# Performance work log

Hardware: AMD Instinct MI355X
Metric: run time of the kernel (lower is better)

## Reference

```python
import jax, jax.numpy as jnp
import numpy as np

NEG_RATIO = 5          # neg_sample_ratio, also k (num_nodes-1 >> ratio)
THRESH = 0.7           # hard_neg_threshold
SMOOTH = 0.1           # label_smoothing
NUM_NODES = 200_000
DIM = 128
B = 1024               # batch size, all labels == 1 (all positives)
FILL_VAL = -1.0e9


def _l2_normalize(x, eps=1e-12):
    # F.normalize(p=2, dim=-1): divide by clamped L2 norm
    n = jnp.sqrt(jnp.sum(x * x, axis=-1, keepdims=True))
    return x / jnp.maximum(n, eps)


def setup_inputs() -> dict:
    key = jax.random.key(0)
    k1, k2, k3, k4 = jax.random.split(key, 4)
    src_nodes = jax.random.randint(k1, (B,), 0, NUM_NODES)
    dst_nodes = jax.random.randint(k2, (B,), 0, NUM_NODES)
    labels = jnp.ones((B,), dtype=jnp.float32)  # all positives -> pos_mask all True
    timestamps = jax.random.uniform(k3, (B,), dtype=jnp.float32)
    memory = jax.random.normal(k4, (NUM_NODES, DIM), dtype=jnp.float32)
    return {
        "src_nodes": src_nodes,
        "dst_nodes": dst_nodes,
        "labels": labels,
        "timestamps": timestamps,
        "memory": memory,
    }


def reference(src_nodes, dst_nodes, labels, timestamps, memory):
    # --- embedding gather + L2 normalize ---
    src_emb = memory[src_nodes]                      # [B, D]
    s = _l2_normalize(src_emb).astype(jnp.float16)   # use_half_precision=True
    c = _l2_normalize(memory).astype(jnp.float16)    # [N, D]

    # --- similarity [B, N], back to fp32 ---
    sim = jnp.matmul(s, c.T).astype(jnp.float32)

    # --- mask out ground-truth dst and below-threshold sims ---
    cols = jnp.arange(NUM_NODES)
    allowed = cols[None, :] != dst_nodes[:, None]    # exclude GT positives
    valid = allowed & (sim > THRESH)
    score = jnp.where(valid, sim, FILL_VAL)

    # --- top-k hard negatives per positive ---
    k = NEG_RATIO  # min(neg_sample_ratio, num_nodes-1)
    topk_vals, topk_idx = jax.lax.top_k(score, k)    # [B, k]
    is_real = (topk_vals > FILL_VAL + 1.0).reshape(-1)  # [B*k]

    # --- fallback random negatives (fixed-shape equivalent of the torch
    #     pack-real-then-pad-random assembly; total count == B*k either way) ---
    rkey = jax.random.key(42)
    rand_dst = jax.random.randint(rkey, (B * k,), 0, NUM_NODES)
    src_rep = jnp.repeat(src_nodes, k)               # [B*k]
    rand_dst = jnp.where(rand_dst == src_rep, (rand_dst + 1) % NUM_NODES, rand_dst)

    final_src = src_rep
    final_dst = jnp.where(is_real, topk_idx.reshape(-1), rand_dst)
    neg_ts = jnp.repeat(timestamps, k)

    # --- assemble augmented batch ---
    new_src = jnp.concatenate([src_nodes, final_src])
    new_dst = jnp.concatenate([dst_nodes, final_dst])
    new_labels = jnp.concatenate([labels, jnp.zeros((B * k,), labels.dtype)])
    new_ts = jnp.concatenate([timestamps, neg_ts])

    # --- label smoothing ---
    new_labels = new_labels * (1.0 - SMOOTH) + (1.0 - new_labels) * SMOOTH

    return new_src, new_dst, new_labels, new_ts, topk_vals
```

## Files before the change

### kernel.cpp

```cpp
#include <hip/hip_runtime.h>

#define NUM_NODES 200000
#define DIM 128
#define BATCH 1024
#define K_NEG 5
#define CAP 16
#define NBLK 250
#define CPB 800
#define TCOL 32
#define NT 25
#define THRESH 0.7f
#define FILL (-1.0e9f)

typedef __attribute__((ext_vector_type(8))) short short8;
typedef __attribute__((ext_vector_type(16))) float f32x16;

__device__ __forceinline__ unsigned short f2bf(float x) {
  unsigned u = __builtin_bit_cast(unsigned, x);
  return (unsigned short)((u + 0x7fffu + ((u >> 16) & 1u)) >> 16);
}

__device__ __forceinline__ void stage16(const void* g, void* l) {
  __builtin_amdgcn_global_load_lds(
      (const __attribute__((address_space(1))) unsigned int*)g,
      (__attribute__((address_space(3))) unsigned int*)l,
      16, 0, 0);
}

__device__ __forceinline__ void tf2x32(unsigned k0, unsigned k1,
                                       unsigned x0, unsigned x1,
                                       unsigned* o0, unsigned* o1) {
  unsigned ks2 = k0 ^ k1 ^ 0x1BD11BDAu;
  unsigned v0 = x0 + k0, v1 = x1 + k1;
#define TFR(r) { v0 += v1; v1 = (v1 << r) | (v1 >> (32 - r)); v1 ^= v0; }
  TFR(13) TFR(15) TFR(26) TFR(6)   v0 += k1;  v1 += ks2 + 1u;
  TFR(17) TFR(29) TFR(16) TFR(24)  v0 += ks2; v1 += k0 + 2u;
  TFR(13) TFR(15) TFR(26) TFR(6)   v0 += k0;  v1 += k1 + 3u;
  TFR(17) TFR(29) TFR(16) TFR(24)  v0 += k1;  v1 += ks2 + 4u;
  TFR(13) TFR(15) TFR(26) TFR(6)   v0 += ks2; v1 += k0 + 5u;
#undef TFR
  *o0 = v0; *o1 = v1;
}

__device__ __forceinline__ unsigned rbits32(unsigned ka, unsigned kb, unsigned m) {
  unsigned o0, o1;
  tf2x32(ka, kb, 0u, m, &o0, &o1);
  return o0 ^ o1;
}

__global__ void prep_kernel(const float* __restrict__ memory,
                            const int* __restrict__ src_nodes,
                            unsigned short* __restrict__ s16f,
                            int* __restrict__ cand_cnt) {
  int tid = threadIdx.x;
  int gid = blockIdx.x * 256 + tid;
  if (gid < BATCH) cand_cnt[gid] = 0;
  int row = blockIdx.x * 4 + (tid >> 6);
  int L = tid & 63;
  int s = src_nodes[row];
  float2 v = ((const float2*)(memory + (size_t)s * DIM))[L];
  float ss = v.x * v.x + v.y * v.y;
#pragma unroll
  for (int off = 32; off > 0; off >>= 1) ss += __shfl_xor(ss, off);
  float inv = 1.0f / fmaxf(sqrtf(ss), 1e-12f);
  unsigned p = (unsigned)f2bf(v.x * inv) | ((unsigned)f2bf(v.y * inv) << 16);
  int ms = row >> 5, l32 = row & 31;
  int c = L >> 2;
  int ks = c >> 1, half = c & 1;
  ((unsigned*)s16f)[(((ms * 8 + ks) * 64) + half * 32 + l32) * 4 + (L & 3)] = p;
}

__global__ __launch_bounds__(512, 2) void sim_scan_kernel(
    const float* __restrict__ memory,
    const unsigned short* __restrict__ s16f,
    const int* __restrict__ dst_nodes,
    int* __restrict__ cand_cnt,
    float* __restrict__ cand_val,
    int* __restrict__ cand_idx) {
  __shared__ char qbuf[8][2048];
  __shared__ unsigned short fragb[2][4096];
  __shared__ float nrmb[2][32];

  int tid = threadIdx.x;
  int wid = tid >> 6;
  int lane = tid & 63;
  int half = lane >> 5;
  int l32 = lane & 31;
  int jb0 = blockIdx.x * CPB;

  int ccol = wid * 4 + (lane & 3);
  int cseg = lane >> 2;

  const char* mb = (const char*)memory;

#define QSTAGE(t) {                                                             \
    const char* g = mb + (size_t)(jb0 + (t) * TCOL + ccol) * 512 + (cseg << 5); \
    stage16(g, &qbuf[wid][0]);                                                  \
    stage16(g + 16, &qbuf[wid][1024]);                                          \
  }

#define QCONVERT(p) {                                                           \
    asm volatile("s_waitcnt vmcnt(0)" ::: "memory");                            \
    __builtin_amdgcn_sched_barrier(0);                                          \
    float4 q0 = *(const float4*)(&qbuf[wid][lane << 4]);                        \
    float4 q1 = *(const float4*)(&qbuf[wid][1024 + (lane << 4)]);               \
    float ss = q0.x * q0.x + q0.y * q0.y + q0.z * q0.z + q0.w * q0.w            \
             + q1.x * q1.x + q1.y * q1.y + q1.z * q1.z + q1.w * q1.w;           \
    ss += __shfl_xor(ss, 4); ss += __shfl_xor(ss, 8);                           \
    ss += __shfl_xor(ss, 16); ss += __shfl_xor(ss, 32);                         \
    short8 f;                                                                   \
    f[0] = (short)f2bf(q0.x); f[1] = (short)f2bf(q0.y);                         \
    f[2] = (short)f2bf(q0.z); f[3] = (short)f2bf(q0.w);                         \
    f[4] = (short)f2bf(q1.x); f[5] = (short)f2bf(q1.y);                         \
    f[6] = (short)f2bf(q1.z); f[7] = (short)f2bf(q1.w);                         \
    *(short8*)((char*)fragb[p] + ((cseg * 32 + (ccol ^ (cseg & 7))) << 4)) = f; \
    if (cseg == 0) nrmb[p][ccol] = fmaxf(sqrtf(ss), 1e-12f);                    \
  }

  QSTAGE(0);
  const short8* __restrict__ af = (const short8*)s16f;
  short8 a[4][8];
#pragma unroll
  for (int m = 0; m < 4; ++m)
#pragma unroll
    for (int ks = 0; ks < 8; ++ks)
      a[m][ks] = af[(((wid * 4 + m) * 8) + ks) * 64 + lane];
  QCONVERT(0);
  __syncthreads();

  f32x16 Z;
#pragma unroll
  for (int i = 0; i < 16; ++i) Z[i] = 0.0f;

  for (int t = 0; t < NT; ++t) {
    int par = t & 1;

    if (t + 1 < NT) QSTAGE(t + 1);

    float nv = nrmb[par][l32];
    float thr = THRESH * nv;
    float invv = 1.0f / nv;
    int gj = jb0 + t * TCOL + l32;
    short8 bf[8];
#pragma unroll
    for (int ks = 0; ks < 8; ++ks) {
      int s0 = 2 * ks + half;
      bf[ks] = *(const short8*)((char*)fragb[par] + ((s0 * 32 + (l32 ^ (s0 & 7))) << 4));
    }

#pragma unroll
    for (int mp = 0; mp < 2; ++mp) {
      f32x16 accA = __builtin_amdgcn_mfma_f32_32x32x16_bf16(a[mp * 2][0], bf[0], Z, 0, 0, 0);
      f32x16 accB = __builtin_amdgcn_mfma_f32_32x32x16_bf16(a[mp * 2 + 1][0], bf[0], Z, 0, 0, 0);
#pragma unroll
      for (int ks = 1; ks < 8; ++ks) {
        accA = __builtin_amdgcn_mfma_f32_32x32x16_bf16(a[mp * 2][ks], bf[ks], accA, 0, 0, 0);
        accB = __builtin_amdgcn_mfma_f32_32x32x16_bf16(a[mp * 2 + 1][ks], bf[ks], accB, 0, 0, 0);
      }
      float mA = accA[0], mB = accB[0];
#pragma unroll
      for (int i = 1; i < 16; ++i) { mA = fmaxf(mA, accA[i]); mB = fmaxf(mB, accB[i]); }
      if (mA > thr || mB > thr) {
#pragma unroll
        for (int e = 0; e < 2; ++e) {
#pragma unroll
          for (int r = 0; r < 16; ++r) {
            float raw = (e == 0) ? accA[r] : accB[r];
            if (raw > thr) {
              int gi = (wid * 4 + mp * 2 + e) * 32 + (r & 3) + 8 * (r >> 2) + 4 * half;
              if (gj != dst_nodes[gi]) {
                int pq = atomicAdd(&cand_cnt[gi], 1);
                if (pq < CAP) {
                  cand_val[gi * CAP + pq] = raw * invv;
                  cand_idx[gi * CAP + pq] = gj;
                }
              }
            }
          }
        }
      }
    }

    if (t + 1 < NT) QCONVERT(par ^ 1);

    __syncthreads();
  }
#undef QSTAGE
#undef QCONVERT
}

__global__ void finalize_kernel(const int* __restrict__ src_nodes,
                                const int* __restrict__ dst_nodes,
                                const float* __restrict__ labels,
                                const float* __restrict__ ts,
                                const int* __restrict__ cand_cnt,
                                const float* __restrict__ cand_val,
                                const int* __restrict__ cand_idx,
                                float* __restrict__ out) {
  int r = blockIdx.x * 256 + threadIdx.x;
  if (r >= BATCH) return;
  const int TOT = BATCH + BATCH * K_NEG;
  int srcv = src_nodes[r];
  float tsv = ts[r];
  out[r] = (float)srcv;
  out[TOT + r] = (float)dst_nodes[r];
  float l = labels[r];
  out[2 * TOT + r] = l * 0.9f + (1.0f - l) * 0.1f;
  out[3 * TOT + r] = tsv;

  int cnt = cand_cnt[r];
  cnt = cnt < CAP ? cnt : CAP;
  float cv[CAP]; int ci[CAP];
  for (int i = 0; i < cnt; ++i) { cv[i] = cand_val[r * CAP + i]; ci[i] = cand_idx[r * CAP + i]; }

  unsigned k1a, k1b, k2a, k2b;
  tf2x32(0u, 42u, 0u, 0u, &k1a, &k1b);
  tf2x32(0u, 42u, 0u, 1u, &k2a, &k2b);

  const unsigned span = 200000u;
  const unsigned mult = 167296u;

  for (int s = 0; s < K_NEG; ++s) {
    int sel = -1;
    for (int i = 0; i < cnt; ++i)
      if (sel < 0 || cv[i] > cv[sel] || (cv[i] == cv[sel] && ci[i] < ci[sel])) sel = i;
    float v = FILL; int idx = 0;
    if (sel >= 0) { v = cv[sel]; idx = ci[sel]; cv[sel] = FILL; ci[sel] = 0x7fffffff; }
    bool is_real = v > (FILL + 1.0f);

    unsigned m = (unsigned)(r * K_NEG + s);
    unsigned hi = rbits32(k1a, k1b, m);
    unsigned lo = rbits32(k2a, k2b, m);
    unsigned off = ((hi % span) * mult + (lo % span)) % span;
    int rd = (int)off;
    if (rd == srcv) rd = (rd + 1) % NUM_NODES;
    int fd = is_real ? idx : rd;

    int mi = (int)m;
    out[BATCH + mi] = (float)srcv;
    out[TOT + BATCH + mi] = (float)fd;
    out[2 * TOT + BATCH + mi] = 0.1f;
    out[3 * TOT + BATCH + mi] = tsv;
    out[4 * TOT + mi] = v;
  }
}

extern "C" void kernel_launch(void* const* d_in, const int* in_sizes, int n_in,
                              void* d_out, int out_size, void* d_ws, size_t ws_size,
                              hipStream_t stream) {
  const int* src = (const int*)d_in[0];
  const int* dst = (const int*)d_in[1];
  const float* labels = (const float*)d_in[2];
  const float* ts = (const float*)d_in[3];
  const float* memory = (const float*)d_in[4];
  float* out = (float*)d_out;

  char* ws = (char*)d_ws;
  unsigned short* s16f = (unsigned short*)ws;
  int* cand_cnt = (int*)(ws + 262144);
  float* cand_val = (float*)(ws + 266240);
  int* cand_idx = (int*)(ws + 331776);

  prep_kernel<<<256, 256, 0, stream>>>(memory, src, s16f, cand_cnt);
  sim_scan_kernel<<<NBLK, 512, 0, stream>>>(memory, s16f, dst, cand_cnt, cand_val, cand_idx);
  finalize_kernel<<<(BATCH + 255) / 256, 256, 0, stream>>>(src, dst, labels, ts,
                                                           cand_cnt, cand_val, cand_idx, out);
}
```

Measured before the change: 183.4 us.

## Batch four column tiles per pipeline phase to deepen prefetch and cut barriers

The similarity scan now stages, converts and multiplies four 32-column tiles per pipeline phase instead of one. Each block therefore has four tiles of memory loads in flight at once, and the number of block-wide barriers and vmcnt waits drops from one per tile to one per group of four. The 25th tile is handled as a tail step. The LDS staging and fragment buffers grow fourfold to about 129 KB per block, which limits each CU to one resident block. With 250 blocks this is roughly one block per CU anyway.

Result: slower. 222.2 us (+21.1%).

```diff
diff --git a/kernel.cpp b/kernel.cpp
--- a/kernel.cpp
+++ b/kernel.cpp
@@ -6,9 +6,8 @@
 #define K_NEG 5
 #define CAP 16
 #define NBLK 250
-#define CPB 800
+#define NTPB 25
 #define TCOL 32
-#define NT 25
 #define THRESH 0.7f
 #define FILL (-1.0e9f)
 
@@ -77,33 +76,32 @@
     int* __restrict__ cand_cnt,
     float* __restrict__ cand_val,
     int* __restrict__ cand_idx) {
-  __shared__ char qbuf[8][2048];
-  __shared__ unsigned short fragb[2][4096];
-  __shared__ float nrmb[2][32];
+  __shared__ char qbuf[8][8192];
+  __shared__ unsigned short fragb[2][16384];
+  __shared__ float nrmb[2][128];
 
   int tid = threadIdx.x;
   int wid = tid >> 6;
   int lane = tid & 63;
   int half = lane >> 5;
   int l32 = lane & 31;
-  int jb0 = blockIdx.x * CPB;
+  int gtb = blockIdx.x * NTPB;
 
   int ccol = wid * 4 + (lane & 3);
   int cseg = lane >> 2;
 
   const char* mb = (const char*)memory;
-
-#define QSTAGE(t) {                                                             \
-    const char* g = mb + (size_t)(jb0 + (t) * TCOL + ccol) * 512 + (cseg << 5); \
-    stage16(g, &qbuf[wid][0]);                                                  \
-    stage16(g + 16, &qbuf[wid][1024]);                                          \
-  }
-
-#define QCONVERT(p) {                                                           \
-    asm volatile("s_waitcnt vmcnt(0)" ::: "memory");                            \
-    __builtin_amdgcn_sched_barrier(0);                                          \
-    float4 q0 = *(const float4*)(&qbuf[wid][lane << 4]);                        \
-    float4 q1 = *(const float4*)(&qbuf[wid][1024 + (lane << 4)]);               \
+  char* qb = &qbuf[wid][0];
+
+#define QSTAGE1(lt, tt) {                                                       \
+    const char* g = mb + (size_t)((gtb + (lt)) * TCOL + ccol) * 512 + (cseg << 5); \
+    stage16(g, qb + (tt) * 2048);                                               \
+    stage16(g + 16, qb + (tt) * 2048 + 1024);                                   \
+  }
+
+#define QCONV1(p2, tt) {                                                        \
+    float4 q0 = *(const float4*)(qb + (tt) * 2048 + (lane << 4));               \
+    float4 q1 = *(const float4*)(qb + (tt) * 2048 + 1024 + (lane << 4));        \
     float ss = q0.x * q0.x + q0.y * q0.y + q0.z * q0.z + q0.w * q0.w            \
              + q1.x * q1.x + q1.y * q1.y + q1.z * q1.z + q1.w * q1.w;           \
     ss += __shfl_xor(ss, 4); ss += __shfl_xor(ss, 8);                           \
@@ -113,11 +111,59 @@
     f[2] = (short)f2bf(q0.z); f[3] = (short)f2bf(q0.w);                         \
     f[4] = (short)f2bf(q1.x); f[5] = (short)f2bf(q1.y);                         \
     f[6] = (short)f2bf(q1.z); f[7] = (short)f2bf(q1.w);                         \
-    *(short8*)((char*)fragb[p] + ((cseg * 32 + (ccol ^ (cseg & 7))) << 4)) = f; \
-    if (cseg == 0) nrmb[p][ccol] = fmaxf(sqrtf(ss), 1e-12f);                    \
-  }
-
-  QSTAGE(0);
+    *(short8*)((char*)fragb[p2] + (tt) * 8192 +                                 \
+               ((cseg * 32 + (ccol ^ (cseg & 7))) << 4)) = f;                   \
+    if (cseg == 0) nrmb[p2][(tt) * 32 + ccol] = fmaxf(sqrtf(ss), 1e-12f);       \
+  }
+
+#define MFMA1(par, tt, lt) {                                                    \
+    float nv = nrmb[par][(tt) * 32 + l32];                                      \
+    float thr = THRESH * nv;                                                    \
+    float invv = 1.0f / nv;                                                     \
+    int gj = (gtb + (lt)) * TCOL + l32;                                         \
+    short8 bf[8];                                                               \
+    _Pragma("unroll")                                                           \
+    for (int ks = 0; ks < 8; ++ks) {                                            \
+      int s0 = 2 * ks + half;                                                   \
+      bf[ks] = *(const short8*)((char*)fragb[par] + (tt) * 8192 +               \
+                                ((s0 * 32 + (l32 ^ (s0 & 7))) << 4));           \
+    }                                                                           \
+    _Pragma("unroll")                                                           \
+    for (int mp = 0; mp < 2; ++mp) {                                            \
+      f32x16 accA = __builtin_amdgcn_mfma_f32_32x32x16_bf16(a[mp*2][0], bf[0], Z, 0, 0, 0); \
+      f32x16 accB = __builtin_amdgcn_mfma_f32_32x32x16_bf16(a[mp*2+1][0], bf[0], Z, 0, 0, 0); \
+      _Pragma("unroll")                                                         \
+      for (int ks = 1; ks < 8; ++ks) {                                          \
+        accA = __builtin_amdgcn_mfma_f32_32x32x16_bf16(a[mp*2][ks], bf[ks], accA, 0, 0, 0); \
+        accB = __builtin_amdgcn_mfma_f32_32x32x16_bf16(a[mp*2+1][ks], bf[ks], accB, 0, 0, 0); \
+      }                                                                         \
+      float mA = accA[0], mB = accB[0];                                         \
+      _Pragma("unroll")                                                         \
+      for (int i2 = 1; i2 < 16; ++i2) { mA = fmaxf(mA, accA[i2]); mB = fmaxf(mB, accB[i2]); } \
+      if (mA > thr || mB > thr) {                                               \
+        _Pragma("unroll")                                                       \
+        for (int e = 0; e < 2; ++e) {                                           \
+          _Pragma("unroll")                                                     \
+          for (int r = 0; r < 16; ++r) {                                        \
+            float raw = (e == 0) ? accA[r] : accB[r];                           \
+            if (raw > thr) {                                                    \
+              int gi = (wid * 4 + mp * 2 + e) * 32 + (r & 3) + 8 * (r >> 2) + 4 * half; \
+              if (gj != dst_nodes[gi]) {                                        \
+                int pq = atomicAdd(&cand_cnt[gi], 1);                           \
+                if (pq < CAP) {                                                 \
+                  cand_val[gi * CAP + pq] = raw * invv;                         \
+                  cand_idx[gi * CAP + pq] = gj;                                 \
+                }                                                               \
+              }                                                                 \
+            }                                                                   \
+          }                                                                     \
+        }                                                                       \
+      }                                                                         \
+    }                                                                           \
+  }
+
+#pragma unroll
+  for (int tt = 0; tt < 4; ++tt) QSTAGE1(tt, tt);
   const short8* __restrict__ af = (const short8*)s16f;
   short8 a[4][8];
 #pragma unroll
@@ -125,68 +171,44 @@
 #pragma unroll
     for (int ks = 0; ks < 8; ++ks)
       a[m][ks] = af[(((wid * 4 + m) * 8) + ks) * 64 + lane];
-  QCONVERT(0);
+  asm volatile("s_waitcnt vmcnt(0)" ::: "memory");
+  __builtin_amdgcn_sched_barrier(0);
+#pragma unroll
+  for (int tt = 0; tt < 4; ++tt) QCONV1(0, tt);
   __syncthreads();
 
   f32x16 Z;
 #pragma unroll
   for (int i = 0; i < 16; ++i) Z[i] = 0.0f;
 
-  for (int t = 0; t < NT; ++t) {
-    int par = t & 1;
-
-    if (t + 1 < NT) QSTAGE(t + 1);
-
-    float nv = nrmb[par][l32];
-    float thr = THRESH * nv;
-    float invv = 1.0f / nv;
-    int gj = jb0 + t * TCOL + l32;
-    short8 bf[8];
-#pragma unroll
-    for (int ks = 0; ks < 8; ++ks) {
-      int s0 = 2 * ks + half;
-      bf[ks] = *(const short8*)((char*)fragb[par] + ((s0 * 32 + (l32 ^ (s0 & 7))) << 4));
+  for (int p = 0; p < 6; ++p) {
+    int par = p & 1;
+    int base = p * 4;
+
+    if (p < 5) {
+#pragma unroll
+      for (int tt = 0; tt < 4; ++tt) QSTAGE1(base + 4 + tt, tt);
+    } else {
+      QSTAGE1(24, 0);
     }
 
-#pragma unroll
-    for (int mp = 0; mp < 2; ++mp) {
-      f32x16 accA = __builtin_amdgcn_mfma_f32_32x32x16_bf16(a[mp * 2][0], bf[0], Z, 0, 0, 0);
-      f32x16 accB = __builtin_amdgcn_mfma_f32_32x32x16_bf16(a[mp * 2 + 1][0], bf[0], Z, 0, 0, 0);
-#pragma unroll
-      for (int ks = 1; ks < 8; ++ks) {
-        accA = __builtin_amdgcn_mfma_f32_32x32x16_bf16(a[mp * 2][ks], bf[ks], accA, 0, 0, 0);
-        accB = __builtin_amdgcn_mfma_f32_32x32x16_bf16(a[mp * 2 + 1][ks], bf[ks], accB, 0, 0, 0);
-      }
-      float mA = accA[0], mB = accB[0];
-#pragma unroll
-      for (int i = 1; i < 16; ++i) { mA = fmaxf(mA, accA[i]); mB = fmaxf(mB, accB[i]); }
-      if (mA > thr || mB > thr) {
-#pragma unroll
-        for (int e = 0; e < 2; ++e) {
-#pragma unroll
-          for (int r = 0; r < 16; ++r) {
-            float raw = (e == 0) ? accA[r] : accB[r];
-            if (raw > thr) {
-              int gi = (wid * 4 + mp * 2 + e) * 32 + (r & 3) + 8 * (r >> 2) + 4 * half;
-              if (gj != dst_nodes[gi]) {
-                int pq = atomicAdd(&cand_cnt[gi], 1);
-                if (pq < CAP) {
-                  cand_val[gi * CAP + pq] = raw * invv;
-                  cand_idx[gi * CAP + pq] = gj;
-                }
-              }
-            }
-          }
-        }
-      }
+    for (int tt = 0; tt < 4; ++tt) MFMA1(par, tt, base + tt);
+
+    asm volatile("s_waitcnt vmcnt(0)" ::: "memory");
+    __builtin_amdgcn_sched_barrier(0);
+    if (p < 5) {
+#pragma unroll
+      for (int tt = 0; tt < 4; ++tt) QCONV1(par ^ 1, tt);
+    } else {
+      QCONV1(par ^ 1, 0);
     }
-
-    if (t + 1 < NT) QCONVERT(par ^ 1);
-
     __syncthreads();
   }
-#undef QSTAGE
-#undef QCONVERT
+
+  MFMA1(0, 0, 24);
+#undef QSTAGE1
+#undef QCONV1
+#undef MFMA1
 }
 
 __global__ void finalize_kernel(const int* __restrict__ src_nodes,
```
